# Kernel optimization log

Measured on AMD Instinct MI355X. Metric: run time of the kernel, lower is better.

## Reference

```python
import jax, jax.numpy as jnp
import numpy as np

DIM = 256
DEPTH = 6
HEADS = 8
DH = DIM // HEADS            # 32
BUCKET = 64
TEMP = 0.75                  # sort-net softmax temperature
FF = 4 * DIM
B, T = 4, 8192


def layernorm(x, g, b, eps=1e-5):
    m = x.mean(-1, keepdims=True)
    v = ((x - m) ** 2).mean(-1, keepdims=True)
    return (x - m) * jax.lax.rsqrt(v + eps) * g + b


def sinkhorn_attn(q, k, v):
    # q,k,v: (bh, t, dh). Bucketed attention with differentiable top-1 bucket routing
    bh, t, dh = q.shape
    nb = t // BUCKET
    bq = q.reshape(bh, nb, BUCKET, dh)
    bk = k.reshape(bh, nb, BUCKET, dh)
    bv = v.reshape(bh, nb, BUCKET, dh)
    # sort net: bucket summaries -> routing matrix R (differentiable_topk, k=1)
    sq = bq.mean(2)                                   # (bh, nb, dh)
    sk = bk.mean(2)
    R = jnp.einsum('bie,bje->bij', sq, sk) * (dh ** -0.5)
    probs = jax.nn.softmax(R / TEMP, axis=-1)
    top = jnp.max(probs, axis=-1, keepdims=True)      # (bh, nb, 1)
    idx = jnp.argmax(probs, axis=-1)                  # (bh, nb)
    Rtop = jax.nn.one_hot(idx, nb, dtype=q.dtype) * top
    # gather routed key/value buckets (weighted by routing prob)
    bk_r = jnp.einsum('bij,bjtd->bitd', Rtop, bk)
    bv_r = jnp.einsum('bij,bjtd->bitd', Rtop, bv)
    K = jnp.concatenate([bk_r, bk], axis=2)           # (bh, nb, 2*BUCKET, dh)
    V = jnp.concatenate([bv_r, bv], axis=2)
    dots = jnp.einsum('buie,buje->buij', bq, K) * (dh ** -0.5)
    attn = jax.nn.softmax(dots, axis=-1)
    out = jnp.einsum('buij,buje->buie', attn, V)
    return out.reshape(bh, t, dh)


def setup_inputs() -> dict:
    key = jax.random.key(0)
    ks = jax.random.split(key, 18)
    s = 0.02
    f32 = jnp.float32
    inp = {
        'x': jax.random.normal(ks[0], (B, DIM, T), f32),
        'pe0': jax.random.normal(ks[1], (T // BUCKET, DIM), f32) * s,
        'pe1': jax.random.normal(ks[2], (BUCKET, DIM), f32) * s,
        'ln1_g': jnp.ones((DEPTH, DIM), f32),
        'ln1_b': jnp.zeros((DEPTH, DIM), f32),
        'Wq': jax.random.normal(ks[3], (DEPTH, DIM, DIM), f32) * s,
        'Wkv': jax.random.normal(ks[4], (DEPTH, DIM, 2 * DIM), f32) * s,
        'Wo': jax.random.normal(ks[5], (DEPTH, DIM, DIM), f32) * s,
        'bo': jnp.zeros((DEPTH, DIM), f32),
        'ln2_g': jnp.ones((DEPTH, DIM), f32),
        'ln2_b': jnp.zeros((DEPTH, DIM), f32),
        'W1': jax.random.normal(ks[6], (DEPTH, DIM, FF), f32) * s,
        'b1': jnp.zeros((DEPTH, FF), f32),
        'W2': jax.random.normal(ks[7], (DEPTH, FF, DIM), f32) * s,
        'b2': jnp.zeros((DEPTH, DIM), f32),
        'gf': jnp.ones((DIM,), f32),
        'bf': jnp.zeros((DIM,), f32),
    }
    return inp


def _forward(x, pe0, pe1, ln1_g, ln1_b, Wq, Wkv, Wo, bo, ln2_g, ln2_b, W1, b1, W2, b2, gf, bf):
    b, _, t = x.shape
    y = jnp.transpose(x, (0, 2, 1))                      # (b, t, dim)
    pos = (pe0[:, None, :] + pe1[None, :, :]).reshape(-1, DIM)[:t]
    y = y + pos

    def split_heads(u):
        return u.reshape(b, t, HEADS, DH).transpose(0, 2, 1, 3).reshape(b * HEADS, t, DH)

    def step(y, p):
        g1, b1_, wq, wkv, wo, bo_, g2, b2_, w1, bb1, w2, bb2 = p
        h = layernorm(y, g1, b1_)
        q = h @ wq
        k, v = jnp.split(h @ wkv, 2, axis=-1)
        o = sinkhorn_attn(split_heads(q), split_heads(k), split_heads(v))
        o = o.reshape(b, HEADS, t, DH).transpose(0, 2, 1, 3).reshape(b, t, DIM)
        y = y + o @ wo + bo_
        h = layernorm(y, g2, b2_)
        y = y + jax.nn.gelu(h @ w1 + bb1, approximate=False) @ w2 + bb2
        return y, None

    y, _ = jax.lax.scan(step, y, (ln1_g, ln1_b, Wq, Wkv, Wo, bo, ln2_g, ln2_b, W1, b1, W2, b2))
    y = layernorm(y, gf, bf)
    return jnp.transpose(y, (0, 2, 1))


def reference(x, pe0, pe1, ln1_g, ln1_b, Wq, Wkv, Wo, bo, ln2_g, ln2_b, W1, b1, W2, b2, gf, bf):
    return _forward(x, pe0, pe1, ln1_g, ln1_b, Wq, Wkv, Wo, bo, ln2_g, ln2_b, W1, b1, W2, b2, gf, bf)
```

## Files before the change

kernel.cpp:

```cpp
#include <hip/hip_runtime.h>
#include <cstdint>
#include <cstddef>

#define T_LEN 8192
#define DIMC  256
#define NBUCK 128
#define BHEAD 32
#define MROWS 32768

typedef __attribute__((ext_vector_type(8))) short bf16x8;
typedef __attribute__((ext_vector_type(4))) float f32x4;

__device__ __forceinline__ ushort f2bf(float x) {
  union { float f; unsigned u; } v; v.f = x;
  unsigned r = v.u + 0x7fffu + ((v.u >> 16) & 1u);
  return (ushort)(r >> 16);
}
__device__ __forceinline__ float bf2f(ushort u) {
  union { unsigned u; float f; } v; v.u = ((unsigned)u) << 16; return v.f;
}

__device__ __forceinline__ void gld16(const void* g, void* l) {
  __builtin_amdgcn_global_load_lds((const __attribute__((address_space(1))) void*)g,
                                   (__attribute__((address_space(3))) void*)l, 16, 0, 0);
}

__device__ __forceinline__ float fast_gelu(float v) {
  float t2 = fmaf(v * v, 0.07135481283f, 1.5957691216f);
  float z  = v * t2;
  float e  = __expf(-z);
  return v * __builtin_amdgcn_rcpf(1.0f + e);
}

__global__ __launch_bounds__(256)
void add_pos_k(const float* __restrict__ x, const float* __restrict__ pe0,
               const float* __restrict__ pe1, float* __restrict__ y) {
  __shared__ float tile[32][33];
  int b  = blockIdx.z;
  int t0 = blockIdx.x * 32;
  int d0 = blockIdx.y * 32;
  int tj = threadIdx.x;
  int di = threadIdx.y;
#pragma unroll
  for (int k = 0; k < 4; k++) {
    int d = d0 + di + k * 8;
    tile[di + k * 8][tj] = x[((size_t)b * DIMC + d) * T_LEN + t0 + tj];
  }
  __syncthreads();
#pragma unroll
  for (int k = 0; k < 4; k++) {
    int t = t0 + di + k * 8;
    int d = d0 + tj;
    y[((size_t)b * T_LEN + t) * DIMC + d] =
        tile[tj][di + k * 8] + pe0[(size_t)(t >> 6) * DIMC + d] + pe1[(size_t)(t & 63) * DIMC + d];
  }
}

__global__ __launch_bounds__(256)
void layernorm_k(const float* __restrict__ x, const float* __restrict__ g,
                 const float* __restrict__ b, ushort* __restrict__ o) {
  int row  = blockIdx.x * 4 + (threadIdx.x >> 6);
  int lane = threadIdx.x & 63;
  const float4* xr = (const float4*)(x + (size_t)row * DIMC);
  float4 v = xr[lane];
  float s  = v.x + v.y + v.z + v.w;
  float s2 = v.x * v.x + v.y * v.y + v.z * v.z + v.w * v.w;
#pragma unroll
  for (int off = 32; off; off >>= 1) {
    s  += __shfl_xor(s, off);
    s2 += __shfl_xor(s2, off);
  }
  float mean = s * (1.0f / 256.0f);
  float var  = s2 * (1.0f / 256.0f) - mean * mean;
  float r    = rsqrtf(var + 1e-5f);
  float4 gv = ((const float4*)g)[lane];
  float4 bv = ((const float4*)b)[lane];
  ushort4 o4;
  o4.x = f2bf((v.x - mean) * r * gv.x + bv.x);
  o4.y = f2bf((v.y - mean) * r * gv.y + bv.y);
  o4.z = f2bf((v.z - mean) * r * gv.z + bv.z);
  o4.w = f2bf((v.w - mean) * r * gv.w + bv.w);
  ((ushort4*)(o + (size_t)row * DIMC))[lane] = o4;
}

__global__ __launch_bounds__(256)
void wt_bf16_k(const float* __restrict__ W, ushort* __restrict__ Wt,
               int K, int N, size_t outStride) {
  __shared__ float t[32][33];
  int l = blockIdx.z;
  const float* Wl = W + (size_t)l * K * N;
  ushort* Wtl = Wt + (size_t)l * outStride;
  int n0 = blockIdx.x * 32, k0 = blockIdx.y * 32;
  int tx = threadIdx.x, ty = threadIdx.y;
#pragma unroll
  for (int p = 0; p < 4; p++)
    t[ty + p * 8][tx] = Wl[(size_t)(k0 + ty + p * 8) * N + n0 + tx];
  __syncthreads();
#pragma unroll
  for (int p = 0; p < 4; p++)
    Wtl[(size_t)(n0 + ty + p * 8) * K + k0 + tx] = f2bf(t[tx][ty + p * 8]);
}

template <int EPI>
__global__ __launch_bounds__(256)
void gemm_bf16(const ushort* __restrict__ A, const ushort* __restrict__ Bt,
               const float* __restrict__ bias, ushort* __restrict__ Cbf,
               int N, int K, int lda, int ldb) {
  __shared__ ushort sm[2][8192];
  int tid = threadIdx.x;
  int w = tid >> 6, lane = tid & 63;
  int bm = blockIdx.x << 7, bn = blockIdx.y << 7;
  int wm = (w >> 1) << 6, wn = (w & 1) << 6;
  int l15 = lane & 15, quad = lane >> 4;

  int off0 = (w << 11) + (lane << 4);
  int r0 = off0 >> 6;
  int r1 = (off0 + 1024) >> 6;
  int swc = (((lane & 3) ^ ((lane >> 3) & 3)) << 3);
  const ushort* ga0 = A + (size_t)(bm + r0) * lda + swc;
  const ushort* ga1 = A + (size_t)(bm + r1) * lda + swc;
  const ushort* gb0 = Bt + (size_t)(bn + r0) * ldb + swc;
  const ushort* gb1 = Bt + (size_t)(bn + r1) * ldb + swc;
  int aoff0 = (w << 10) + 0;
  int aoff1 = aoff0 + 512;
  int boff0 = 4096 + (w << 10);
  int boff1 = boff0 + 512;

  int sq = quad ^ ((l15 >> 1) & 3);

  f32x4 acc[4][4];
#pragma unroll
  for (int i = 0; i < 4; i++)
#pragma unroll
    for (int j = 0; j < 4; j++) {
      f32x4 z = {0.f, 0.f, 0.f, 0.f};
      acc[i][j] = z;
    }

  gld16(ga0, &sm[0][aoff0]);
  gld16(ga1, &sm[0][aoff1]);
  gld16(gb0, &sm[0][boff0]);
  gld16(gb1, &sm[0][boff1]);
  __syncthreads();

  int cur = 0;
  for (int k0 = 0; k0 < K; k0 += 32) {
    if (k0 + 32 < K) {
      ushort* S = sm[cur ^ 1];
      gld16(ga0 + k0 + 32, S + aoff0);
      gld16(ga1 + k0 + 32, S + aoff1);
      gld16(gb0 + k0 + 32, S + boff0);
      gld16(gb1 + k0 + 32, S + boff1);
    }
    const ushort* Sc = sm[cur];
    bf16x8 aF[4], bF[4];
#pragma unroll
    for (int i = 0; i < 4; i++)
      aF[i] = *(const bf16x8*)(Sc + ((wm + (i << 4) + l15) << 5) + (sq << 3));
#pragma unroll
    for (int j = 0; j < 4; j++)
      bF[j] = *(const bf16x8*)(Sc + 4096 + ((wn + (j << 4) + l15) << 5) + (sq << 3));
#pragma unroll
    for (int i = 0; i < 4; i++)
#pragma unroll
      for (int j = 0; j < 4; j++)
        acc[i][j] = __builtin_amdgcn_mfma_f32_16x16x32_bf16(aF[i], bF[j], acc[i][j], 0, 0, 0);
    __syncthreads();
    cur ^= 1;
  }

  ushort (*eb)[16][66] = (ushort(*)[16][66])&sm[0][0];
  float bvj[4];
  if (EPI == 1) {
#pragma unroll
    for (int j = 0; j < 4; j++) bvj[j] = bias[bn + wn + (j << 4) + l15];
  }
#pragma unroll
  for (int i = 0; i < 4; i++) {
#pragma unroll
    for (int j = 0; j < 4; j++) {
#pragma unroll
      for (int r = 0; r < 4; r++) {
        float v = acc[i][j][r];
        if (EPI == 1) v = fast_gelu(v + bvj[j]);
        eb[w][(quad << 2) + r][(j << 4) + l15] = f2bf(v);
      }
    }
#pragma unroll
    for (int h = 0; h < 2; h++) {
      int chunk = (h << 6) + lane;
      int row = chunk >> 3, c8 = (chunk & 7) << 3;
      bf16x8 vv = *(const bf16x8*)&eb[w][row][c8];
      *(bf16x8*)&Cbf[(size_t)(bm + wm + (i << 4) + row) * N + bn + wn + c8] = vv;
    }
  }
}

template <int FINAL>
__global__ __launch_bounds__(256)
void oproj_ln_k(const ushort* __restrict__ A, const ushort* __restrict__ Bt,
                const float* __restrict__ bias, float* __restrict__ y,
                const float* __restrict__ g, const float* __restrict__ b,
                ushort* __restrict__ obf, int K, int lda) {
  __shared__ ushort smem[20480];
  __shared__ float red[2][64][2];
  __shared__ float stat[64][2];
  int tid = threadIdx.x;
  int wid = tid >> 6, lane = tid & 63;
  int l15 = lane & 15, quad = lane >> 4;
  int bm = blockIdx.x << 6;
  int wm = (wid >> 1) << 5;
  int wn = (wid & 1) << 7;

  int swc = (((tid & 3) ^ ((tid >> 3) & 3)) << 3);
  const ushort* gaA = A + (size_t)(bm + (tid >> 2)) * lda + swc;
  const ushort* gaB[4];
#pragma unroll
  for (int p = 0; p < 4; p++) {
    int u = (p << 8) + tid;
    gaB[p] = Bt + (size_t)(u >> 2) * K + swc;
  }
  int lAoff = tid << 3;
  int lBoff[4];
#pragma unroll
  for (int p = 0; p < 4; p++) lBoff[p] = 2048 + (((p << 8) + tid) << 3);

  int sq = quad ^ ((l15 >> 1) & 3);

  f32x4 acc[2][8];
#pragma unroll
  for (int i = 0; i < 2; i++)
#pragma unroll
    for (int j = 0; j < 8; j++) {
      f32x4 z = {0.f, 0.f, 0.f, 0.f};
      acc[i][j] = z;
    }

  gld16(gaA, smem + lAoff);
#pragma unroll
  for (int p = 0; p < 4; p++) gld16(gaB[p], smem + lBoff[p]);
  __syncthreads();

  int cur = 0;
  for (int k0 = 0; k0 < K; k0 += 32) {
    if (k0 + 32 < K) {
      ushort* S = smem + ((cur ^ 1) ? 10240 : 0);
      gld16(gaA + k0 + 32, S + lAoff);
#pragma unroll
      for (int p = 0; p < 4; p++) gld16(gaB[p] + k0 + 32, S + lBoff[p]);
    }
    const ushort* Sc = smem + (cur ? 10240 : 0);
    bf16x8 aF[2];
#pragma unroll
    for (int i = 0; i < 2; i++)
      aF[i] = *(const bf16x8*)(Sc + ((wm + (i << 4) + l15) << 5) + (sq << 3));
#pragma unroll
    for (int j = 0; j < 8; j++) {
      bf16x8 bF = *(const bf16x8*)(Sc + 2048 + ((wn + (j << 4) + l15) << 5) + (sq << 3));
#pragma unroll
      for (int i = 0; i < 2; i++)
        acc[i][j] = __builtin_amdgcn_mfma_f32_16x16x32_bf16(aF[i], bF, acc[i][j], 0, 0, 0);
    }
    __syncthreads();
    cur ^= 1;
  }

  float bc[8];
#pragma unroll
  for (int j = 0; j < 8; j++) bc[j] = bias[wn + (j << 4) + l15];
  float s1v[2][4], s2v[2][4];
#pragma unroll
  for (int i = 0; i < 2; i++)
#pragma unroll
    for (int r = 0; r < 4; r++) {
      int row = bm + wm + (i << 4) + (quad << 2) + r;
      float s1 = 0.f, s2 = 0.f;
#pragma unroll
      for (int j = 0; j < 8; j++) {
        size_t idx = (size_t)row * 256 + wn + (j << 4) + l15;
        float v = acc[i][j][r] + bc[j] + y[idx];
        acc[i][j][r] = v;
        if (!FINAL) y[idx] = v;
        s1 += v;
        s2 += v * v;
      }
      s1v[i][r] = s1;
      s2v[i][r] = s2;
    }
#pragma unroll
  for (int off = 1; off < 16; off <<= 1)
#pragma unroll
    for (int i = 0; i < 2; i++)
#pragma unroll
      for (int r = 0; r < 4; r++) {
        s1v[i][r] += __shfl_xor(s1v[i][r], off);
        s2v[i][r] += __shfl_xor(s2v[i][r], off);
      }
  if (l15 == 0) {
#pragma unroll
    for (int i = 0; i < 2; i++)
#pragma unroll
      for (int r = 0; r < 4; r++) {
        int lr = wm + (i << 4) + (quad << 2) + r;
        red[wid & 1][lr][0] = s1v[i][r];
        red[wid & 1][lr][1] = s2v[i][r];
      }
  }
  __syncthreads();
  if (tid < 64) {
    float s  = red[0][tid][0] + red[1][tid][0];
    float s2 = red[0][tid][1] + red[1][tid][1];
    float mean = s * (1.0f / 256.0f);
    float var  = s2 * (1.0f / 256.0f) - mean * mean;
    stat[tid][0] = mean;
    stat[tid][1] = rsqrtf(var + 1e-5f);
  }
  __syncthreads();

  if (FINAL) {
#pragma unroll
    for (int j = 0; j < 8; j++) {
      int col = wn + (j << 4) + l15;
      float gc = g[col], bc2 = b[col];
#pragma unroll
      for (int i = 0; i < 2; i++)
#pragma unroll
        for (int r = 0; r < 4; r++) {
          int lr = wm + (i << 4) + (quad << 2) + r;
          float o = (acc[i][j][r] - stat[lr][0]) * stat[lr][1] * gc + bc2;
          y[(size_t)(bm + lr) * 256 + col] = o;
        }
    }
  } else {
    ushort (*eb)[264] = (ushort(*)[264])smem;
#pragma unroll
    for (int j = 0; j < 8; j++) {
      int col = wn + (j << 4) + l15;
      float gc = g[col], bc2 = b[col];
#pragma unroll
      for (int i = 0; i < 2; i++)
#pragma unroll
        for (int r = 0; r < 4; r++) {
          int lr = wm + (i << 4) + (quad << 2) + r;
          float o = (acc[i][j][r] - stat[lr][0]) * stat[lr][1] * gc + bc2;
          eb[lr][col] = f2bf(o);
        }
    }
    __syncthreads();
#pragma unroll
    for (int h = 0; h < 8; h++) {
      int chunk = (h << 8) + tid;
      int row = chunk >> 5, c8 = (chunk & 31) << 3;
      bf16x8 vv = *(const bf16x8*)&eb[row][c8];
      *(bf16x8*)&obf[(size_t)(bm + row) * 256 + c8] = vv;
    }
  }
}

__global__ __launch_bounds__(64)
void summary_k(const ushort* __restrict__ qkv,
               float* __restrict__ sq, float* __restrict__ sk) {
  int blk = blockIdx.x;
  int bh = blk >> 7, ib = blk & 127;
  int b = bh >> 3, h = bh & 7;
  int lane = threadIdx.x;
  int d = lane & 31;
  bool isK = lane >= 32;
  size_t base = ((size_t)b * T_LEN + (size_t)ib * 64) * 768 + (isK ? 256 : 0) + h * 32 + d;
  float s = 0.f;
#pragma unroll 8
  for (int t = 0; t < 64; t++) s += bf2f(qkv[base + (size_t)t * 768]);
  s *= (1.0f / 64.0f);
  float* dst = isK ? sk : sq;
  dst[((size_t)bh * NBUCK + ib) * 32 + d] = s;
}

__global__ __launch_bounds__(64)
void route_k(const float* __restrict__ sq, const float* __restrict__ sk,
             int* __restrict__ ridx, float* __restrict__ rw) {
  int blk = blockIdx.x;
  int bh = blk >> 7, ib = blk & 127;
  int lane = threadIdx.x;
  const float* qrow = sq + ((size_t)bh * NBUCK + ib) * 32;
  const float* k0 = sk + ((size_t)bh * NBUCK + lane) * 32;
  const float* k1 = k0 + 64 * 32;
  float s0 = 0.f, s1 = 0.f;
#pragma unroll
  for (int d = 0; d < 32; d++) {
    float qd = qrow[d];
    s0 += qd * k0[d];
    s1 += qd * k1[d];
  }
  const float sc = 0.17677669529663687f * (4.0f / 3.0f);
  float L0 = s0 * sc, L1 = s1 * sc;
  float m = fmaxf(L0, L1);
#pragma unroll
  for (int off = 32; off; off >>= 1) m = fmaxf(m, __shfl_xor(m, off));
  float Z = expf(L0 - m) + expf(L1 - m);
#pragma unroll
  for (int off = 32; off; off >>= 1) Z += __shfl_xor(Z, off);
  float mv = (L1 > L0) ? L1 : L0;
  int mj = (L1 > L0) ? lane + 64 : lane;
#pragma unroll
  for (int off = 32; off; off >>= 1) {
    float ov = __shfl_xor(mv, off);
    int oj = __shfl_xor(mj, off);
    if (ov > mv || (ov == mv && oj < mj)) { mv = ov; mj = oj; }
  }
  if (lane == 0) {
    ridx[blk] = mj;
    rw[blk] = 1.0f / Z;
  }
}

__global__ __launch_bounds__(256)
void attn_mfma_k(const ushort* __restrict__ qkv,
                 const int* __restrict__ ridx, const float* __restrict__ rw,
                 ushort* __restrict__ o) {
  __shared__ ushort Qs[64][40];
  __shared__ ushort Ks[128][40];
  __shared__ ushort Vt[32][136];
  __shared__ ushort Ps[4][16][136];
  int blk = blockIdx.x;
  int bh = blk >> 7, ib = blk & 127;
  int b = bh >> 3, h = bh & 7;
  int tid = threadIdx.x;
  int jr = ridx[blk];
  float w = rw[blk];
  {
    int r = tid >> 2, c = (tid & 3) << 3;
    const ushort* src = qkv + ((size_t)b * T_LEN + (size_t)ib * 64 + r) * 768 + h * 32 + c;
    *(bf16x8*)&Qs[r][c] = *(const bf16x8*)src;
  }
#pragma unroll
  for (int p = 0; p < 2; p++) {
    int idx = tid + (p << 8);
    int r = idx >> 2, c = (idx & 3) << 3;
    int srcb = (r < 64) ? jr : ib;
    int tt = r & 63;
    const ushort* src = qkv + ((size_t)b * T_LEN + (size_t)srcb * 64 + tt) * 768 + 256 + h * 32 + c;
    *(bf16x8*)&Ks[r][c] = *(const bf16x8*)src;
  }
  {
    int tok = tid >> 1, d0 = (tid & 1) << 4;
    int srcb = (tok < 64) ? jr : ib;
    int tt = tok & 63;
    const ushort* src = qkv + ((size_t)b * T_LEN + (size_t)srcb * 64 + tt) * 768 + 512 + h * 32 + d0;
    bf16x8 v0 = *(const bf16x8*)src;
    bf16x8 v1 = *(const bf16x8*)(src + 8);
#pragma unroll
    for (int j = 0; j < 8; j++) {
      Vt[d0 + j][tok] = (ushort)v0[j];
      Vt[d0 + 8 + j][tok] = (ushort)v1[j];
    }
  }
  __syncthreads();
  int wid = tid >> 6, lane = tid & 63, l15 = lane & 15, quad = lane >> 4;
  bf16x8 aQ = *(const bf16x8*)&Qs[(wid << 4) + l15][quad << 3];
  f32x4 sf[8];
#pragma unroll
  for (int jn = 0; jn < 8; jn++) {
    bf16x8 bK = *(const bf16x8*)&Ks[(jn << 4) + l15][quad << 3];
    f32x4 z = {0.f, 0.f, 0.f, 0.f};
    sf[jn] = __builtin_amdgcn_mfma_f32_16x16x32_bf16(aQ, bK, z, 0, 0, 0);
  }
  const float sc = 0.17677669529663687f;
#pragma unroll
  for (int jn = 0; jn < 8; jn++) {
    float mult = (jn < 4) ? w * sc : sc;
#pragma unroll
    for (int r = 0; r < 4; r++) sf[jn][r] *= mult;
  }
  float mx[4], sm[4], inv[4];
#pragma unroll
  for (int r = 0; r < 4; r++) {
    float m = sf[0][r];
#pragma unroll
    for (int jn = 1; jn < 8; jn++) m = fmaxf(m, sf[jn][r]);
    mx[r] = m;
  }
#pragma unroll
  for (int off = 1; off < 16; off <<= 1)
#pragma unroll
    for (int r = 0; r < 4; r++) mx[r] = fmaxf(mx[r], __shfl_xor(mx[r], off));
#pragma unroll
  for (int r = 0; r < 4; r++) sm[r] = 0.f;
#pragma unroll
  for (int jn = 0; jn < 8; jn++)
#pragma unroll
    for (int r = 0; r < 4; r++) {
      sf[jn][r] = __expf(sf[jn][r] - mx[r]);
      sm[r] += sf[jn][r];
    }
#pragma unroll
  for (int off = 1; off < 16; off <<= 1)
#pragma unroll
    for (int r = 0; r < 4; r++) sm[r] += __shfl_xor(sm[r], off);
#pragma unroll
  for (int r = 0; r < 4; r++) inv[r] = __builtin_amdgcn_rcpf(sm[r]);
#pragma unroll
  for (int jn = 0; jn < 8; jn++) {
    float ws2 = (jn < 4) ? w : 1.f;
#pragma unroll
    for (int r = 0; r < 4; r++)
      Ps[wid][(quad << 2) + r][(jn << 4) + l15] = f2bf(sf[jn][r] * inv[r] * ws2);
  }
  f32x4 of[2];
#pragma unroll
  for (int nd = 0; nd < 2; nd++) { f32x4 z = {0.f, 0.f, 0.f, 0.f}; of[nd] = z; }
#pragma unroll
  for (int kk = 0; kk < 4; kk++) {
    bf16x8 aP = *(const bf16x8*)&Ps[wid][l15][(kk << 5) + (quad << 3)];
#pragma unroll
    for (int nd = 0; nd < 2; nd++) {
      bf16x8 bV = *(const bf16x8*)&Vt[(nd << 4) + l15][(kk << 5) + (quad << 3)];
      of[nd] = __builtin_amdgcn_mfma_f32_16x16x32_bf16(aP, bV, of[nd], 0, 0, 0);
    }
  }
  ushort* obase = o + ((size_t)b * T_LEN + (size_t)ib * 64 + (wid << 4) + (quad << 2)) * 256 + h * 32 + l15;
#pragma unroll
  for (int nd = 0; nd < 2; nd++)
#pragma unroll
    for (int r = 0; r < 4; r++)
      obase[(size_t)r * 256 + (nd << 4)] = f2bf(of[nd][r]);
}

__global__ __launch_bounds__(256)
void transpose_out_k(const float* __restrict__ yln, float* __restrict__ out) {
  __shared__ float tile[32][33];
  int b  = blockIdx.z;
  int t0 = blockIdx.x * 32;
  int d0 = blockIdx.y * 32;
  int tx = threadIdx.x;
  int ty = threadIdx.y;
#pragma unroll
  for (int k = 0; k < 4; k++) {
    int t = t0 + ty + k * 8;
    tile[ty + k * 8][tx] = yln[((size_t)b * T_LEN + t) * DIMC + d0 + tx];
  }
  __syncthreads();
#pragma unroll
  for (int k = 0; k < 4; k++) {
    int d = d0 + ty + k * 8;
    out[((size_t)b * DIMC + d) * T_LEN + t0 + tx] = tile[tx][ty + k * 8];
  }
}

extern "C" void kernel_launch(void* const* d_in, const int* in_sizes, int n_in,
                              void* d_out, int out_size, void* d_ws, size_t ws_size,
                              hipStream_t stream) {
  const float* x     = (const float*)d_in[0];
  const float* pe0   = (const float*)d_in[1];
  const float* pe1   = (const float*)d_in[2];
  const float* ln1_g = (const float*)d_in[3];
  const float* ln1_b = (const float*)d_in[4];
  const float* Wq    = (const float*)d_in[5];
  const float* Wkv   = (const float*)d_in[6];
  const float* Wo    = (const float*)d_in[7];
  const float* bo    = (const float*)d_in[8];
  const float* ln2_g = (const float*)d_in[9];
  const float* ln2_b = (const float*)d_in[10];
  const float* W1    = (const float*)d_in[11];
  const float* b1    = (const float*)d_in[12];
  const float* W2    = (const float*)d_in[13];
  const float* b2    = (const float*)d_in[14];
  const float* gf    = (const float*)d_in[15];
  const float* bfp   = (const float*)d_in[16];
  float* out = (float*)d_out;

  const int M = MROWS;
  float*  y    = (float*)d_ws;
  ushort* qkv  = (ushort*)(y + (size_t)M * 256);
  ushort* bufA = qkv + (size_t)M * 768;
  ushort* bufB = bufA + (size_t)M * 256;
  ushort* wbf  = bufB + (size_t)M * 256;
  float*  sqb  = (float*)(wbf + (size_t)6 * 786432);
  float*  skb  = sqb + 131072;
  float*  rwb  = skb + 131072;
  int*    rib  = (int*)(rwb + 4096);
  ushort* ffbf = qkv;

  dim3 tb(32, 8);
  wt_bf16_k<<<dim3(8, 8, 6),  tb, 0, stream>>>(Wq,  wbf + 0,      256, 256,  786432);
  wt_bf16_k<<<dim3(16, 8, 6), tb, 0, stream>>>(Wkv, wbf + 65536,  256, 512,  786432);
  wt_bf16_k<<<dim3(8, 8, 6),  tb, 0, stream>>>(Wo,  wbf + 196608, 256, 256,  786432);
  wt_bf16_k<<<dim3(32, 8, 6), tb, 0, stream>>>(W1,  wbf + 262144, 256, 1024, 786432);
  wt_bf16_k<<<dim3(8, 32, 6), tb, 0, stream>>>(W2,  wbf + 524288, 1024, 256, 786432);

  add_pos_k<<<dim3(T_LEN / 32, DIMC / 32, 4), tb, 0, stream>>>(x, pe0, pe1, y);
  layernorm_k<<<M / 4, 256, 0, stream>>>(y, ln1_g, ln1_b, bufB);

  for (int l = 0; l < 6; l++) {
    const ushort* wl    = wbf + (size_t)l * 786432;
    const ushort* wqkvT = wl;
    const ushort* woT   = wl + 196608;
    const ushort* w1T   = wl + 262144;
    const ushort* w2T   = wl + 524288;

    gemm_bf16<0><<<dim3(M / 128, 6), 256, 0, stream>>>(bufB, wqkvT, nullptr, qkv, 768, 256, 256, 256);
    summary_k<<<BHEAD * NBUCK, 64, 0, stream>>>(qkv, sqb, skb);
    route_k<<<BHEAD * NBUCK, 64, 0, stream>>>(sqb, skb, rib, rwb);
    attn_mfma_k<<<BHEAD * NBUCK, 256, 0, stream>>>(qkv, rib, rwb, bufA);
    oproj_ln_k<0><<<M / 64, 256, 0, stream>>>(bufA, woT, bo + l * 256, y,
                                              ln2_g + l * 256, ln2_b + l * 256,
                                              bufB, 256, 256);
    gemm_bf16<1><<<dim3(M / 128, 8), 256, 0, stream>>>(bufB, w1T, b1 + l * 1024, ffbf, 1024, 256, 256, 256);
    if (l < 5) {
      oproj_ln_k<0><<<M / 64, 256, 0, stream>>>(ffbf, w2T, b2 + l * 256, y,
                                                ln1_g + (l + 1) * 256, ln1_b + (l + 1) * 256,
                                                bufB, 1024, 1024);
    } else {
      oproj_ln_k<1><<<M / 64, 256, 0, stream>>>(ffbf, w2T, b2 + l * 256, y,
                                                gf, bfp, nullptr, 1024, 1024);
    }
  }

  transpose_out_k<<<dim3(T_LEN / 32, DIMC / 32, 4), tb, 0, stream>>>(y, out);

  (void)in_sizes; (void)n_in; (void)out_size; (void)ws_size;
}
```

Baseline: 1.124 ms.

## Enlarge GEMM tiles to 128x256 and oproj-LN tiles to 128 rows with BK=64

```diff
diff --git a/kernel.cpp b/kernel.cpp
--- a/kernel.cpp
+++ b/kernel.cpp
@@ -102,83 +102,90 @@
 }
 
 template <int EPI>
-__global__ __launch_bounds__(256)
+__global__ __launch_bounds__(256, 2)
 void gemm_bf16(const ushort* __restrict__ A, const ushort* __restrict__ Bt,
                const float* __restrict__ bias, ushort* __restrict__ Cbf,
                int N, int K, int lda, int ldb) {
-  __shared__ ushort sm[2][8192];
+  __shared__ ushort sm[2][12288];
   int tid = threadIdx.x;
   int w = tid >> 6, lane = tid & 63;
-  int bm = blockIdx.x << 7, bn = blockIdx.y << 7;
-  int wm = (w >> 1) << 6, wn = (w & 1) << 6;
+  int bm = blockIdx.x << 7, bn = blockIdx.y << 8;
+  int wm = (w >> 1) << 6;
+  int wn = (w & 1) << 7;
   int l15 = lane & 15, quad = lane >> 4;
 
-  int off0 = (w << 11) + (lane << 4);
-  int r0 = off0 >> 6;
-  int r1 = (off0 + 1024) >> 6;
-  int swc = (((lane & 3) ^ ((lane >> 3) & 3)) << 3);
-  const ushort* ga0 = A + (size_t)(bm + r0) * lda + swc;
-  const ushort* ga1 = A + (size_t)(bm + r1) * lda + swc;
-  const ushort* gb0 = Bt + (size_t)(bn + r0) * ldb + swc;
-  const ushort* gb1 = Bt + (size_t)(bn + r1) * ldb + swc;
-  int aoff0 = (w << 10) + 0;
-  int aoff1 = aoff0 + 512;
-  int boff0 = 4096 + (w << 10);
-  int boff1 = boff0 + 512;
+  const ushort* gA[2]; int lA[2];
+#pragma unroll
+  for (int p = 0; p < 2; p++) {
+    int u = tid + (p << 8);
+    int row = u >> 2;
+    int swc = (((u & 3) ^ ((row >> 1) & 3)) << 3);
+    gA[p] = A + (size_t)(bm + row) * lda + swc;
+    lA[p] = u << 3;
+  }
+  const ushort* gB[4]; int lB[4];
+#pragma unroll
+  for (int p = 0; p < 4; p++) {
+    int u = tid + (p << 8);
+    int row = u >> 2;
+    int swc = (((u & 3) ^ ((row >> 1) & 3)) << 3);
+    gB[p] = Bt + (size_t)(bn + row) * ldb + swc;
+    lB[p] = 4096 + (u << 3);
+  }
 
   int sq = quad ^ ((l15 >> 1) & 3);
 
-  f32x4 acc[4][4];
+  f32x4 acc[4][8];
 #pragma unroll
   for (int i = 0; i < 4; i++)
 #pragma unroll
-    for (int j = 0; j < 4; j++) {
+    for (int j = 0; j < 8; j++) {
       f32x4 z = {0.f, 0.f, 0.f, 0.f};
       acc[i][j] = z;
     }
 
-  gld16(ga0, &sm[0][aoff0]);
-  gld16(ga1, &sm[0][aoff1]);
-  gld16(gb0, &sm[0][boff0]);
-  gld16(gb1, &sm[0][boff1]);
+#pragma unroll
+  for (int p = 0; p < 2; p++) gld16(gA[p], &sm[0][lA[p]]);
+#pragma unroll
+  for (int p = 0; p < 4; p++) gld16(gB[p], &sm[0][lB[p]]);
   __syncthreads();
 
   int cur = 0;
   for (int k0 = 0; k0 < K; k0 += 32) {
     if (k0 + 32 < K) {
       ushort* S = sm[cur ^ 1];
-      gld16(ga0 + k0 + 32, S + aoff0);
-      gld16(ga1 + k0 + 32, S + aoff1);
-      gld16(gb0 + k0 + 32, S + boff0);
-      gld16(gb1 + k0 + 32, S + boff1);
+#pragma unroll
+      for (int p = 0; p < 2; p++) gld16(gA[p] + k0 + 32, S + lA[p]);
+#pragma unroll
+      for (int p = 0; p < 4; p++) gld16(gB[p] + k0 + 32, S + lB[p]);
     }
     const ushort* Sc = sm[cur];
-    bf16x8 aF[4], bF[4];
+    bf16x8 aF[4], bF[8];
 #pragma unroll
     for (int i = 0; i < 4; i++)
       aF[i] = *(const bf16x8*)(Sc + ((wm + (i << 4) + l15) << 5) + (sq << 3));
 #pragma unroll
-    for (int j = 0; j < 4; j++)
+    for (int j = 0; j < 8; j++)
       bF[j] = *(const bf16x8*)(Sc + 4096 + ((wn + (j << 4) + l15) << 5) + (sq << 3));
 #pragma unroll
     for (int i = 0; i < 4; i++)
 #pragma unroll
-      for (int j = 0; j < 4; j++)
+      for (int j = 0; j < 8; j++)
         acc[i][j] = __builtin_amdgcn_mfma_f32_16x16x32_bf16(aF[i], bF[j], acc[i][j], 0, 0, 0);
     __syncthreads();
     cur ^= 1;
   }
 
-  ushort (*eb)[16][66] = (ushort(*)[16][66])&sm[0][0];
-  float bvj[4];
+  ushort (*eb)[16][136] = (ushort(*)[16][136])&sm[0][0];
+  float bvj[8];
   if (EPI == 1) {
 #pragma unroll
-    for (int j = 0; j < 4; j++) bvj[j] = bias[bn + wn + (j << 4) + l15];
+    for (int j = 0; j < 8; j++) bvj[j] = bias[bn + wn + (j << 4) + l15];
   }
 #pragma unroll
   for (int i = 0; i < 4; i++) {
 #pragma unroll
-    for (int j = 0; j < 4; j++) {
+    for (int j = 0; j < 8; j++) {
 #pragma unroll
       for (int r = 0; r < 4; r++) {
         float v = acc[i][j][r];
@@ -187,9 +194,9 @@
       }
     }
 #pragma unroll
-    for (int h = 0; h < 2; h++) {
+    for (int h = 0; h < 4; h++) {
       int chunk = (h << 6) + lane;
-      int row = chunk >> 3, c8 = (chunk & 7) << 3;
+      int row = chunk >> 4, c8 = (chunk & 15) << 3;
       bf16x8 vv = *(const bf16x8*)&eb[w][row][c8];
       *(bf16x8*)&Cbf[(size_t)(bm + wm + (i << 4) + row) * N + bn + wn + c8] = vv;
     }
@@ -197,69 +204,78 @@
 }
 
 template <int FINAL>
-__global__ __launch_bounds__(256)
+__global__ __launch_bounds__(256, 1)
 void oproj_ln_k(const ushort* __restrict__ A, const ushort* __restrict__ Bt,
                 const float* __restrict__ bias, float* __restrict__ y,
                 const float* __restrict__ g, const float* __restrict__ b,
                 ushort* __restrict__ obf, int K, int lda) {
-  __shared__ ushort smem[20480];
-  __shared__ float red[2][64][2];
-  __shared__ float stat[64][2];
+  __shared__ ushort smem[49152];
+  __shared__ float red[2][128][2];
+  __shared__ float stat[128][2];
   int tid = threadIdx.x;
   int wid = tid >> 6, lane = tid & 63;
   int l15 = lane & 15, quad = lane >> 4;
-  int bm = blockIdx.x << 6;
-  int wm = (wid >> 1) << 5;
+  int bm = blockIdx.x << 7;
+  int wm = (wid >> 1) << 6;
   int wn = (wid & 1) << 7;
 
-  int swc = (((tid & 3) ^ ((tid >> 3) & 3)) << 3);
-  const ushort* gaA = A + (size_t)(bm + (tid >> 2)) * lda + swc;
-  const ushort* gaB[4];
+  const ushort* gA[4]; int lA[4];
 #pragma unroll
   for (int p = 0; p < 4; p++) {
-    int u = (p << 8) + tid;
-    gaB[p] = Bt + (size_t)(u >> 2) * K + swc;
-  }
-  int lAoff = tid << 3;
-  int lBoff[4];
-#pragma unroll
-  for (int p = 0; p < 4; p++) lBoff[p] = 2048 + (((p << 8) + tid) << 3);
-
-  int sq = quad ^ ((l15 >> 1) & 3);
-
-  f32x4 acc[2][8];
-#pragma unroll
-  for (int i = 0; i < 2; i++)
+    int u = tid + (p << 8);
+    int row = u >> 3, ch = u & 7;
+    gA[p] = A + (size_t)(bm + row) * lda + ((ch ^ (row & 7)) << 3);
+    lA[p] = u << 3;
+  }
+  const ushort* gB[8]; int lB[8];
+#pragma unroll
+  for (int p = 0; p < 8; p++) {
+    int u = tid + (p << 8);
+    int row = u >> 3, ch = u & 7;
+    gB[p] = Bt + (size_t)row * K + ((ch ^ (row & 7)) << 3);
+    lB[p] = 8192 + (u << 3);
+  }
+
+  f32x4 acc[4][8];
+#pragma unroll
+  for (int i = 0; i < 4; i++)
 #pragma unroll
     for (int j = 0; j < 8; j++) {
       f32x4 z = {0.f, 0.f, 0.f, 0.f};
       acc[i][j] = z;
     }
 
-  gld16(gaA, smem + lAoff);
-#pragma unroll
-  for (int p = 0; p < 4; p++) gld16(gaB[p], smem + lBoff[p]);
+#pragma unroll
+  for (int p = 0; p < 4; p++) gld16(gA[p], smem + lA[p]);
+#pragma unroll
+  for (int p = 0; p < 8; p++) gld16(gB[p], smem + lB[p]);
   __syncthreads();
 
   int cur = 0;
-  for (int k0 = 0; k0 < K; k0 += 32) {
-    if (k0 + 32 < K) {
-      ushort* S = smem + ((cur ^ 1) ? 10240 : 0);
-      gld16(gaA + k0 + 32, S + lAoff);
-#pragma unroll
-      for (int p = 0; p < 4; p++) gld16(gaB[p] + k0 + 32, S + lBoff[p]);
-    }
-    const ushort* Sc = smem + (cur ? 10240 : 0);
-    bf16x8 aF[2];
-#pragma unroll
-    for (int i = 0; i < 2; i++)
-      aF[i] = *(const bf16x8*)(Sc + ((wm + (i << 4) + l15) << 5) + (sq << 3));
-#pragma unroll
-    for (int j = 0; j < 8; j++) {
-      bf16x8 bF = *(const bf16x8*)(Sc + 2048 + ((wn + (j << 4) + l15) << 5) + (sq << 3));
-#pragma unroll
-      for (int i = 0; i < 2; i++)
-        acc[i][j] = __builtin_amdgcn_mfma_f32_16x16x32_bf16(aF[i], bF, acc[i][j], 0, 0, 0);
+  for (int k0 = 0; k0 < K; k0 += 64) {
+    if (k0 + 64 < K) {
+      ushort* S = smem + ((cur ^ 1) ? 24576 : 0);
+#pragma unroll
+      for (int p = 0; p < 4; p++) gld16(gA[p] + k0 + 64, S + lA[p]);
+#pragma unroll
+      for (int p = 0; p < 8; p++) gld16(gB[p] + k0 + 64, S + lB[p]);
+    }
+    const ushort* Sc = smem + (cur ? 24576 : 0);
+#pragma unroll
+    for (int s = 0; s < 2; s++) {
+      int chs = (((s << 2) + quad) ^ (l15 & 7)) << 3;
+      bf16x8 aF[4], bF[8];
+#pragma unroll
+      for (int i = 0; i < 4; i++)
+        aF[i] = *(const bf16x8*)(Sc + ((wm + (i << 4) + l15) << 6) + chs);
+#pragma unroll
+      for (int j = 0; j < 8; j++)
+        bF[j] = *(const bf16x8*)(Sc + 8192 + ((wn + (j << 4) + l15) << 6) + chs);
+#pragma unroll
+      for (int i = 0; i < 4; i++)
+#pragma unroll
+        for (int j = 0; j < 8; j++)
+          acc[i][j] = __builtin_amdgcn_mfma_f32_16x16x32_bf16(aF[i], bF[j], acc[i][j], 0, 0, 0);
     }
     __syncthreads();
     cur ^= 1;
@@ -268,9 +284,9 @@
   float bc[8];
 #pragma unroll
   for (int j = 0; j < 8; j++) bc[j] = bias[wn + (j << 4) + l15];
-  float s1v[2][4], s2v[2][4];
-#pragma unroll
-  for (int i = 0; i < 2; i++)
+  float s1v[4][4], s2v[4][4];
+#pragma unroll
+  for (int i = 0; i < 4; i++)
 #pragma unroll
     for (int r = 0; r < 4; r++) {
       int row = bm + wm + (i << 4) + (quad << 2) + r;
@@ -290,7 +306,7 @@
 #pragma unroll
   for (int off = 1; off < 16; off <<= 1)
 #pragma unroll
-    for (int i = 0; i < 2; i++)
+    for (int i = 0; i < 4; i++)
 #pragma unroll
       for (int r = 0; r < 4; r++) {
         s1v[i][r] += __shfl_xor(s1v[i][r], off);
@@ -298,7 +314,7 @@
       }
   if (l15 == 0) {
 #pragma unroll
-    for (int i = 0; i < 2; i++)
+    for (int i = 0; i < 4; i++)
 #pragma unroll
       for (int r = 0; r < 4; r++) {
         int lr = wm + (i << 4) + (quad << 2) + r;
@@ -307,7 +323,7 @@
       }
   }
   __syncthreads();
-  if (tid < 64) {
+  if (tid < 128) {
     float s  = red[0][tid][0] + red[1][tid][0];
     float s2 = red[0][tid][1] + red[1][tid][1];
     float mean = s * (1.0f / 256.0f);
@@ -323,7 +339,7 @@
       int col = wn + (j << 4) + l15;
       float gc = g[col], bc2 = b[col];
 #pragma unroll
-      for (int i = 0; i < 2; i++)
+      for (int i = 0; i < 4; i++)
 #pragma unroll
         for (int r = 0; r < 4; r++) {
           int lr = wm + (i << 4) + (quad << 2) + r;
@@ -338,7 +354,7 @@
       int col = wn + (j << 4) + l15;
       float gc = g[col], bc2 = b[col];
 #pragma unroll
-      for (int i = 0; i < 2; i++)
+      for (int i = 0; i < 4; i++)
 #pragma unroll
         for (int r = 0; r < 4; r++) {
           int lr = wm + (i << 4) + (quad << 2) + r;
@@ -348,7 +364,7 @@
     }
     __syncthreads();
 #pragma unroll
-    for (int h = 0; h < 8; h++) {
+    for (int h = 0; h < 16; h++) {
       int chunk = (h << 8) + tid;
       int row = chunk >> 5, c8 = (chunk & 31) << 3;
       bf16x8 vv = *(const bf16x8*)&eb[row][c8];
@@ -597,21 +613,21 @@
     const ushort* w1T   = wl + 262144;
     const ushort* w2T   = wl + 524288;
 
-    gemm_bf16<0><<<dim3(M / 128, 6), 256, 0, stream>>>(bufB, wqkvT, nullptr, qkv, 768, 256, 256, 256);
+    gemm_bf16<0><<<dim3(M / 128, 3), 256, 0, stream>>>(bufB, wqkvT, nullptr, qkv, 768, 256, 256, 256);
     summary_k<<<BHEAD * NBUCK, 64, 0, stream>>>(qkv, sqb, skb);
     route_k<<<BHEAD * NBUCK, 64, 0, stream>>>(sqb, skb, rib, rwb);
     attn_mfma_k<<<BHEAD * NBUCK, 256, 0, stream>>>(qkv, rib, rwb, bufA);
-    oproj_ln_k<0><<<M / 64, 256, 0, stream>>>(bufA, woT, bo + l * 256, y,
-                                              ln2_g + l * 256, ln2_b + l * 256,
-                                              bufB, 256, 256);
-    gemm_bf16<1><<<dim3(M / 128, 8), 256, 0, stream>>>(bufB, w1T, b1 + l * 1024, ffbf, 1024, 256, 256, 256);
+    oproj_ln_k<0><<<M / 128, 256, 0, stream>>>(bufA, woT, bo + l * 256, y,
+                                               ln2_g + l * 256, ln2_b + l * 256,
+                                               bufB, 256, 256);
+    gemm_bf16<1><<<dim3(M / 128, 4), 256, 0, stream>>>(bufB, w1T, b1 + l * 1024, ffbf, 1024, 256, 256, 256);
     if (l < 5) {
-      oproj_ln_k<0><<<M / 64, 256, 0, stream>>>(ffbf, w2T, b2 + l * 256, y,
-                                                ln1_g + (l + 1) * 256, ln1_b + (l + 1) * 256,
-                                                bufB, 1024, 1024);
+      oproj_ln_k<0><<<M / 128, 256, 0, stream>>>(ffbf, w2T, b2 + l * 256, y,
+                                                 ln1_g + (l + 1) * 256, ln1_b + (l + 1) * 256,
+                                                 bufB, 1024, 1024);
     } else {
-      oproj_ln_k<1><<<M / 64, 256, 0, stream>>>(ffbf, w2T, b2 + l * 256, y,
-                                                gf, bfp, nullptr, 1024, 1024);
+      oproj_ln_k<1><<<M / 128, 256, 0, stream>>>(ffbf, w2T, b2 + l * 256, y,
+                                                 gf, bfp, nullptr, 1024, 1024);
     }
   }
 
```

New measurement: 1.174 ms. 4.5% more time.

## Triple-buffer LDS in GEMM kernels with partial vmcnt waits

Applied to the files above, without the earlier changes.

```diff
diff --git a/kernel.cpp b/kernel.cpp
--- a/kernel.cpp
+++ b/kernel.cpp
@@ -24,6 +24,10 @@
   __builtin_amdgcn_global_load_lds((const __attribute__((address_space(1))) void*)g,
                                    (__attribute__((address_space(3))) void*)l, 16, 0, 0);
 }
+
+#define WAITCNT5 asm volatile("s_waitcnt vmcnt(5) lgkmcnt(0)" ::: "memory")
+#define WAITCNT4 asm volatile("s_waitcnt vmcnt(4) lgkmcnt(0)" ::: "memory")
+#define WAITCNT0 asm volatile("s_waitcnt vmcnt(0) lgkmcnt(0)" ::: "memory")
 
 __device__ __forceinline__ float fast_gelu(float v) {
   float t2 = fmaf(v * v, 0.07135481283f, 1.5957691216f);
@@ -106,7 +110,7 @@
 void gemm_bf16(const ushort* __restrict__ A, const ushort* __restrict__ Bt,
                const float* __restrict__ bias, ushort* __restrict__ Cbf,
                int N, int K, int lda, int ldb) {
-  __shared__ ushort sm[2][8192];
+  __shared__ ushort sm[3][8192];
   int tid = threadIdx.x;
   int w = tid >> 6, lane = tid & 63;
   int bm = blockIdx.x << 7, bn = blockIdx.y << 7;
@@ -121,7 +125,7 @@
   const ushort* ga1 = A + (size_t)(bm + r1) * lda + swc;
   const ushort* gb0 = Bt + (size_t)(bn + r0) * ldb + swc;
   const ushort* gb1 = Bt + (size_t)(bn + r1) * ldb + swc;
-  int aoff0 = (w << 10) + 0;
+  int aoff0 = (w << 10);
   int aoff1 = aoff0 + 512;
   int boff0 = 4096 + (w << 10);
   int boff1 = boff0 + 512;
@@ -137,20 +141,33 @@
       acc[i][j] = z;
     }
 
+  const int T = K >> 5;
   gld16(ga0, &sm[0][aoff0]);
   gld16(ga1, &sm[0][aoff1]);
   gld16(gb0, &sm[0][boff0]);
   gld16(gb1, &sm[0][boff1]);
-  __syncthreads();
+  if (T > 1) {
+    gld16(ga0 + 32, &sm[1][aoff0]);
+    gld16(ga1 + 32, &sm[1][aoff1]);
+    gld16(gb0 + 32, &sm[1][boff0]);
+    gld16(gb1 + 32, &sm[1][boff1]);
+    WAITCNT4;
+  } else {
+    WAITCNT0;
+  }
+  __builtin_amdgcn_s_barrier();
 
   int cur = 0;
-  for (int k0 = 0; k0 < K; k0 += 32) {
-    if (k0 + 32 < K) {
-      ushort* S = sm[cur ^ 1];
-      gld16(ga0 + k0 + 32, S + aoff0);
-      gld16(ga1 + k0 + 32, S + aoff1);
-      gld16(gb0 + k0 + 32, S + boff0);
-      gld16(gb1 + k0 + 32, S + boff1);
+  for (int t = 0; t < T; t++) {
+    bool pf = (t + 2 < T);
+    if (pf) {
+      int nb = cur + 2; if (nb >= 3) nb -= 3;
+      ushort* S = sm[nb];
+      int k0 = (t + 2) << 5;
+      gld16(ga0 + k0, S + aoff0);
+      gld16(ga1 + k0, S + aoff1);
+      gld16(gb0 + k0, S + boff0);
+      gld16(gb1 + k0, S + boff1);
     }
     const ushort* Sc = sm[cur];
     bf16x8 aF[4], bF[4];
@@ -165,8 +182,9 @@
 #pragma unroll
       for (int j = 0; j < 4; j++)
         acc[i][j] = __builtin_amdgcn_mfma_f32_16x16x32_bf16(aF[i], bF[j], acc[i][j], 0, 0, 0);
-    __syncthreads();
-    cur ^= 1;
+    if (pf) { WAITCNT4; } else { WAITCNT0; }
+    __builtin_amdgcn_s_barrier();
+    cur++; if (cur >= 3) cur = 0;
   }
 
   ushort (*eb)[16][66] = (ushort(*)[16][66])&sm[0][0];
@@ -202,7 +220,7 @@
                 const float* __restrict__ bias, float* __restrict__ y,
                 const float* __restrict__ g, const float* __restrict__ b,
                 ushort* __restrict__ obf, int K, int lda) {
-  __shared__ ushort smem[20480];
+  __shared__ ushort smem[30720];
   __shared__ float red[2][64][2];
   __shared__ float stat[64][2];
   int tid = threadIdx.x;
@@ -236,20 +254,32 @@
       acc[i][j] = z;
     }
 
+  const int T = K >> 5;
   gld16(gaA, smem + lAoff);
 #pragma unroll
   for (int p = 0; p < 4; p++) gld16(gaB[p], smem + lBoff[p]);
-  __syncthreads();
+  if (T > 1) {
+    gld16(gaA + 32, smem + 10240 + lAoff);
+#pragma unroll
+    for (int p = 0; p < 4; p++) gld16(gaB[p] + 32, smem + 10240 + lBoff[p]);
+    WAITCNT5;
+  } else {
+    WAITCNT0;
+  }
+  __builtin_amdgcn_s_barrier();
 
   int cur = 0;
-  for (int k0 = 0; k0 < K; k0 += 32) {
-    if (k0 + 32 < K) {
-      ushort* S = smem + ((cur ^ 1) ? 10240 : 0);
-      gld16(gaA + k0 + 32, S + lAoff);
-#pragma unroll
-      for (int p = 0; p < 4; p++) gld16(gaB[p] + k0 + 32, S + lBoff[p]);
-    }
-    const ushort* Sc = smem + (cur ? 10240 : 0);
+  for (int t = 0; t < T; t++) {
+    bool pf = (t + 2 < T);
+    if (pf) {
+      int nb = cur + 2; if (nb >= 3) nb -= 3;
+      ushort* S = smem + nb * 10240;
+      int k0 = (t + 2) << 5;
+      gld16(gaA + k0, S + lAoff);
+#pragma unroll
+      for (int p = 0; p < 4; p++) gld16(gaB[p] + k0, S + lBoff[p]);
+    }
+    const ushort* Sc = smem + cur * 10240;
     bf16x8 aF[2];
 #pragma unroll
     for (int i = 0; i < 2; i++)
@@ -261,8 +291,9 @@
       for (int i = 0; i < 2; i++)
         acc[i][j] = __builtin_amdgcn_mfma_f32_16x16x32_bf16(aF[i], bF, acc[i][j], 0, 0, 0);
     }
-    __syncthreads();
-    cur ^= 1;
+    if (pf) { WAITCNT5; } else { WAITCNT0; }
+    __builtin_amdgcn_s_barrier();
+    cur++; if (cur >= 3) cur = 0;
   }
 
   float bc[8];
```

Result: no change. 1.131 ms (+0.6%).

## Use 512-thread blocks for fused projection+layernorm and move barrier after prefetch

Applied to the files above, without the earlier changes.

```diff
diff --git a/kernel.cpp b/kernel.cpp
--- a/kernel.cpp
+++ b/kernel.cpp
@@ -121,7 +121,7 @@
   const ushort* ga1 = A + (size_t)(bm + r1) * lda + swc;
   const ushort* gb0 = Bt + (size_t)(bn + r0) * ldb + swc;
   const ushort* gb1 = Bt + (size_t)(bn + r1) * ldb + swc;
-  int aoff0 = (w << 10) + 0;
+  int aoff0 = (w << 10);
   int aoff1 = aoff0 + 512;
   int boff0 = 4096 + (w << 10);
   int boff1 = boff0 + 512;
@@ -141,7 +141,6 @@
   gld16(ga1, &sm[0][aoff1]);
   gld16(gb0, &sm[0][boff0]);
   gld16(gb1, &sm[0][boff1]);
-  __syncthreads();
 
   int cur = 0;
   for (int k0 = 0; k0 < K; k0 += 32) {
@@ -152,6 +151,7 @@
       gld16(gb0 + k0 + 32, S + boff0);
       gld16(gb1 + k0 + 32, S + boff1);
     }
+    __syncthreads();
     const ushort* Sc = sm[cur];
     bf16x8 aF[4], bF[4];
 #pragma unroll
@@ -197,77 +197,78 @@
 }
 
 template <int FINAL>
-__global__ __launch_bounds__(256)
+__global__ __launch_bounds__(512)
 void oproj_ln_k(const ushort* __restrict__ A, const ushort* __restrict__ Bt,
                 const float* __restrict__ bias, float* __restrict__ y,
                 const float* __restrict__ g, const float* __restrict__ b,
                 ushort* __restrict__ obf, int K, int lda) {
   __shared__ ushort smem[20480];
-  __shared__ float red[2][64][2];
+  __shared__ float red[4][64][2];
   __shared__ float stat[64][2];
   int tid = threadIdx.x;
   int wid = tid >> 6, lane = tid & 63;
   int l15 = lane & 15, quad = lane >> 4;
   int bm = blockIdx.x << 6;
-  int wm = (wid >> 1) << 5;
-  int wn = (wid & 1) << 7;
-
-  int swc = (((tid & 3) ^ ((tid >> 3) & 3)) << 3);
-  const ushort* gaA = A + (size_t)(bm + (tid >> 2)) * lda + swc;
-  const ushort* gaB[4];
-#pragma unroll
-  for (int p = 0; p < 4; p++) {
-    int u = (p << 8) + tid;
-    gaB[p] = Bt + (size_t)(u >> 2) * K + swc;
-  }
+  int wm = (wid >> 2) << 5;
+  int wn = (wid & 3) << 6;
+
+  const ushort* gaB[2]; int lBoff[2];
+#pragma unroll
+  for (int p = 0; p < 2; p++) {
+    int u = tid + (p << 9);
+    int row = u >> 2, ch = u & 3;
+    gaB[p] = Bt + (size_t)row * K + ((ch ^ ((row >> 1) & 3)) << 3);
+    lBoff[p] = 2048 + (u << 3);
+  }
+  bool doA = (tid < 256);
+  const ushort* gaA = A + (size_t)(bm + (tid >> 2)) * lda +
+                      (((tid & 3) ^ ((tid >> 3) & 3)) << 3);
   int lAoff = tid << 3;
-  int lBoff[4];
-#pragma unroll
-  for (int p = 0; p < 4; p++) lBoff[p] = 2048 + (((p << 8) + tid) << 3);
 
   int sq = quad ^ ((l15 >> 1) & 3);
 
-  f32x4 acc[2][8];
+  f32x4 acc[2][4];
 #pragma unroll
   for (int i = 0; i < 2; i++)
 #pragma unroll
-    for (int j = 0; j < 8; j++) {
+    for (int j = 0; j < 4; j++) {
       f32x4 z = {0.f, 0.f, 0.f, 0.f};
       acc[i][j] = z;
     }
 
-  gld16(gaA, smem + lAoff);
-#pragma unroll
-  for (int p = 0; p < 4; p++) gld16(gaB[p], smem + lBoff[p]);
-  __syncthreads();
+  if (doA) gld16(gaA, smem + lAoff);
+#pragma unroll
+  for (int p = 0; p < 2; p++) gld16(gaB[p], smem + lBoff[p]);
 
   int cur = 0;
   for (int k0 = 0; k0 < K; k0 += 32) {
     if (k0 + 32 < K) {
       ushort* S = smem + ((cur ^ 1) ? 10240 : 0);
-      gld16(gaA + k0 + 32, S + lAoff);
-#pragma unroll
-      for (int p = 0; p < 4; p++) gld16(gaB[p] + k0 + 32, S + lBoff[p]);
-    }
+      if (doA) gld16(gaA + k0 + 32, S + lAoff);
+#pragma unroll
+      for (int p = 0; p < 2; p++) gld16(gaB[p] + k0 + 32, S + lBoff[p]);
+    }
+    __syncthreads();
     const ushort* Sc = smem + (cur ? 10240 : 0);
-    bf16x8 aF[2];
+    bf16x8 aF[2], bF[4];
 #pragma unroll
     for (int i = 0; i < 2; i++)
       aF[i] = *(const bf16x8*)(Sc + ((wm + (i << 4) + l15) << 5) + (sq << 3));
 #pragma unroll
-    for (int j = 0; j < 8; j++) {
-      bf16x8 bF = *(const bf16x8*)(Sc + 2048 + ((wn + (j << 4) + l15) << 5) + (sq << 3));
-#pragma unroll
-      for (int i = 0; i < 2; i++)
-        acc[i][j] = __builtin_amdgcn_mfma_f32_16x16x32_bf16(aF[i], bF, acc[i][j], 0, 0, 0);
-    }
+    for (int j = 0; j < 4; j++)
+      bF[j] = *(const bf16x8*)(Sc + 2048 + ((wn + (j << 4) + l15) << 5) + (sq << 3));
+#pragma unroll
+    for (int i = 0; i < 2; i++)
+#pragma unroll
+      for (int j = 0; j < 4; j++)
+        acc[i][j] = __builtin_amdgcn_mfma_f32_16x16x32_bf16(aF[i], bF[j], acc[i][j], 0, 0, 0);
     __syncthreads();
     cur ^= 1;
   }
 
-  float bc[8];
-#pragma unroll
-  for (int j = 0; j < 8; j++) bc[j] = bias[wn + (j << 4) + l15];
+  float bc[4];
+#pragma unroll
+  for (int j = 0; j < 4; j++) bc[j] = bias[wn + (j << 4) + l15];
   float s1v[2][4], s2v[2][4];
 #pragma unroll
   for (int i = 0; i < 2; i++)
@@ -276,7 +277,7 @@
       int row = bm + wm + (i << 4) + (quad << 2) + r;
       float s1 = 0.f, s2 = 0.f;
 #pragma unroll
-      for (int j = 0; j < 8; j++) {
+      for (int j = 0; j < 4; j++) {
         size_t idx = (size_t)row * 256 + wn + (j << 4) + l15;
         float v = acc[i][j][r] + bc[j] + y[idx];
         acc[i][j][r] = v;
@@ -302,14 +303,14 @@
 #pragma unroll
       for (int r = 0; r < 4; r++) {
         int lr = wm + (i << 4) + (quad << 2) + r;
-        red[wid & 1][lr][0] = s1v[i][r];
-        red[wid & 1][lr][1] = s2v[i][r];
+        red[wid & 3][lr][0] = s1v[i][r];
+        red[wid & 3][lr][1] = s2v[i][r];
       }
   }
   __syncthreads();
   if (tid < 64) {
-    float s  = red[0][tid][0] + red[1][tid][0];
-    float s2 = red[0][tid][1] + red[1][tid][1];
+    float s  = red[0][tid][0] + red[1][tid][0] + red[2][tid][0] + red[3][tid][0];
+    float s2 = red[0][tid][1] + red[1][tid][1] + red[2][tid][1] + red[3][tid][1];
     float mean = s * (1.0f / 256.0f);
     float var  = s2 * (1.0f / 256.0f) - mean * mean;
     stat[tid][0] = mean;
@@ -319,7 +320,7 @@
 
   if (FINAL) {
 #pragma unroll
-    for (int j = 0; j < 8; j++) {
+    for (int j = 0; j < 4; j++) {
       int col = wn + (j << 4) + l15;
       float gc = g[col], bc2 = b[col];
 #pragma unroll
@@ -334,7 +335,7 @@
   } else {
     ushort (*eb)[264] = (ushort(*)[264])smem;
 #pragma unroll
-    for (int j = 0; j < 8; j++) {
+    for (int j = 0; j < 4; j++) {
       int col = wn + (j << 4) + l15;
       float gc = g[col], bc2 = b[col];
 #pragma unroll
@@ -348,8 +349,8 @@
     }
     __syncthreads();
 #pragma unroll
-    for (int h = 0; h < 8; h++) {
-      int chunk = (h << 8) + tid;
+    for (int h = 0; h < 4; h++) {
+      int chunk = (h << 9) + tid;
       int row = chunk >> 5, c8 = (chunk & 31) << 3;
       bf16x8 vv = *(const bf16x8*)&eb[row][c8];
       *(bf16x8*)&obf[(size_t)(bm + row) * 256 + c8] = vv;
@@ -601,16 +602,16 @@
     summary_k<<<BHEAD * NBUCK, 64, 0, stream>>>(qkv, sqb, skb);
     route_k<<<BHEAD * NBUCK, 64, 0, stream>>>(sqb, skb, rib, rwb);
     attn_mfma_k<<<BHEAD * NBUCK, 256, 0, stream>>>(qkv, rib, rwb, bufA);
-    oproj_ln_k<0><<<M / 64, 256, 0, stream>>>(bufA, woT, bo + l * 256, y,
+    oproj_ln_k<0><<<M / 64, 512, 0, stream>>>(bufA, woT, bo + l * 256, y,
                                               ln2_g + l * 256, ln2_b + l * 256,
                                               bufB, 256, 256);
     gemm_bf16<1><<<dim3(M / 128, 8), 256, 0, stream>>>(bufB, w1T, b1 + l * 1024, ffbf, 1024, 256, 256, 256);
     if (l < 5) {
-      oproj_ln_k<0><<<M / 64, 256, 0, stream>>>(ffbf, w2T, b2 + l * 256, y,
+      oproj_ln_k<0><<<M / 64, 512, 0, stream>>>(ffbf, w2T, b2 + l * 256, y,
                                                 ln1_g + (l + 1) * 256, ln1_b + (l + 1) * 256,
                                                 bufB, 1024, 1024);
     } else {
-      oproj_ln_k<1><<<M / 64, 256, 0, stream>>>(ffbf, w2T, b2 + l * 256, y,
+      oproj_ln_k<1><<<M / 64, 512, 0, stream>>>(ffbf, w2T, b2 + l * 256, y,
                                                 gf, bfp, nullptr, 1024, 1024);
     }
   }
```

New measurement: 1.140 ms. No clear change (+1.4%).
